# Performance work log

Hardware: AMD Instinct MI355X
Metric: run time of the kernel (lower is better)

## Reference

```python
import jax, jax.numpy as jnp
import numpy as np

DIM = 512
NUM_HEADS = 16
WS = 8  # window_size
N = WS * WS
B = 1024


def get_relative_index(h, w):
    coords_h = np.arange(h)[:, None].repeat(w, axis=1)
    coords_w = np.arange(w)[None, :].repeat(h, axis=0)
    coords = np.stack([coords_h, coords_w], axis=-1).reshape(-1, 2)  # [N,2]
    rel = coords[:, None, :] - coords[None, :, :]
    rel = rel + np.array([h - 1, w - 1])
    rel[:, :, 0] *= 2 * w - 1
    return rel.sum(-1).astype(np.int32)  # [N,N]


def setup_inputs() -> dict:
    key = jax.random.key(0)
    ks = jax.random.split(key, 6)
    table_size = (2 * WS - 1) * (2 * WS - 1)  # 225
    return {
        "x": jax.random.normal(ks[0], (B, N, DIM), dtype=jnp.float32),
        "qkv_weight": jax.random.normal(ks[1], (3 * DIM, DIM), dtype=jnp.float32) * 0.02,
        "qkv_bias": jax.random.normal(ks[2], (3 * DIM,), dtype=jnp.float32) * 0.02,
        "proj_weight": jax.random.normal(ks[3], (DIM, DIM), dtype=jnp.float32) * 0.02,
        "proj_bias": jax.random.normal(ks[4], (DIM,), dtype=jnp.float32) * 0.02,
        "relative_table": jax.random.normal(ks[5], (table_size, 2 * NUM_HEADS), dtype=jnp.float32) * 0.02,
        "relative_index": jnp.asarray(get_relative_index(WS, WS)),
    }


def reference(x, qkv_weight, qkv_bias, proj_weight, proj_bias, relative_table, relative_index):
    B_, n, C = x.shape
    H = NUM_HEADS
    hd = C // H
    scale = hd ** -0.5
    # qkv projection: [B,N,3C] -> [3,B,H,N,hd]
    qkv = (x @ qkv_weight.T + qkv_bias).reshape(B_, n, 3, H, hd).transpose(2, 0, 3, 1, 4)
    q, k, v = qkv[0], qkv[1], qkv[2]
    attn = jnp.einsum("bhnd,bhmd->bhnm", q * scale, k)  # [B,H,N,N]
    # learned relative-position bias + post-softmax scale
    params = relative_table[relative_index.reshape(-1)].reshape(n, n, 2 * H)
    params = params.transpose(2, 0, 1)  # [2H,N,N]
    rel_bias, rel_scale = params[:H], params[H:]
    attn = jax.nn.softmax(attn + rel_bias[None], axis=-1)
    attn = attn * rel_scale[None]
    out = jnp.einsum("bhnm,bhmd->bhnd", attn, v)
    out = out.transpose(0, 2, 1, 3).reshape(B_, n, C)
    return out @ proj_weight.T + proj_bias
```

## Files before the change

### kernel.cpp

```cpp
#include <hip/hip_runtime.h>

typedef unsigned short u16;
typedef unsigned int   u32;
typedef __attribute__((ext_vector_type(8))) short bf16x8;
typedef __attribute__((ext_vector_type(4))) float f32x4;

#define SCALE 0.17677669529663687f

__device__ __forceinline__ u16 f2bf(float f){
  u32 x = __float_as_uint(f);
  x += 0x7fffu + ((x >> 16) & 1u);
  return (u16)(x >> 16);
}
__device__ __forceinline__ float bf2f(u16 u){
  return __uint_as_float(((u32)u) << 16);
}


__global__ void prep_kernel(const float* __restrict__ qkvw, const float* __restrict__ projw,
                            const float* __restrict__ table, const int* __restrict__ relidx,
                            u16* __restrict__ qkvw_b, u16* __restrict__ projw_b,
                            u16* __restrict__ biasT, u16* __restrict__ scaleT){
  int i = blockIdx.x * 256 + threadIdx.x;
  if (i < 786432) {
    qkvw_b[i] = f2bf(qkvw[i]);
  } else if (i < 1048576) {
    int j = i - 786432; projw_b[j] = f2bf(projw[j]);
  } else if (i < 1114112) {
    int j = i - 1048576; int h = j >> 12, rc = j & 4095;
    int idx = relidx[rc];
    biasT [h*4096 + rc] = f2bf(table[idx*32 + h]);
    scaleT[h*4096 + rc] = f2bf(table[idx*32 + 16 + h]);
  }
}

__global__ void xconv_kernel(const float* __restrict__ x, u16* __restrict__ xb){
  size_t i = (size_t)blockIdx.x * 256 + threadIdx.x;
  const float4* xp = (const float4*)x;
  float4 a = xp[2*i], b = xp[2*i+1];
  union { u16 u[8]; uint4 v; } o;
  o.u[0]=f2bf(a.x); o.u[1]=f2bf(a.y); o.u[2]=f2bf(a.z); o.u[3]=f2bf(a.w);
  o.u[4]=f2bf(b.x); o.u[5]=f2bf(b.y); o.u[6]=f2bf(b.z); o.u[7]=f2bf(b.w);
  *(uint4*)(xb + 8*i) = o.v;
}

template<int EPI>
__global__ __launch_bounds__(512, 2) void gemm_kernel(
    const u16* __restrict__ A, const u16* __restrict__ W,
    const float* __restrict__ bias, void* __restrict__ outp, const int NT)
{
  __shared__ u16 lds[3][24576];
  const int tid = threadIdx.x, lane = tid & 63, wid = tid >> 6;
  const int wave_base = tid & ~63;

  const int cpx = gridDim.x >> 3;
  const int bid = (blockIdx.x & 7) * cpx + (blockIdx.x >> 3);
  const int mt = bid / NT, nt = bid % NT;
  const size_t m0 = (size_t)mt * 128;
  const int n0 = nt * 256;
  const int wm = wid >> 2, wn = wid & 3;
  const int NCOL = (EPI == 0) ? 1536 : 512;

  const f32x4 z = {0.f, 0.f, 0.f, 0.f};
  f32x4 acc[4][4];
#pragma unroll
  for (int i = 0; i < 4; i++)
#pragma unroll
    for (int j = 0; j < 4; j++) acc[i][j] = z;

  auto stage = [&](int ch){
    const int slot = ch % 3;
    const int kb = ch * 128;
    u16* base = &lds[slot][0];
#pragma unroll
    for (int c = 0; c < 2; ++c){
      const int t = c*512 + tid;
      const int row = t >> 3, sl = t & 7;
      const char* ga = (const char*)A + (m0 + row)*1024 + kb + ((sl ^ (row & 7)) << 4);
      u16* la = base + (size_t)(c*512 + wave_base)*8;
      __builtin_amdgcn_global_load_lds((const __attribute__((address_space(1))) u32*)ga,
                                       (__attribute__((address_space(3))) u32*)la, 16, 0, 0);
    }
#pragma unroll
    for (int c = 0; c < 4; ++c){
      const int t = c*512 + tid;
      const int col = t >> 3, sl = t & 7;
      const char* gb = (const char*)W + (size_t)(n0 + col)*1024 + kb + ((sl ^ (col & 7)) << 4);
      u16* lb = base + 8192 + (size_t)(c*512 + wave_base)*8;
      __builtin_amdgcn_global_load_lds((const __attribute__((address_space(1))) u32*)gb,
                                       (__attribute__((address_space(3))) u32*)lb, 16, 0, 0);
    }
  };

  auto compute = [&](int ch){
    const int slot = ch % 3;
    const u16* As = &lds[slot][0];
    const u16* Bs = &lds[slot][8192];
    bf16x8 af[2][4], bfr[2][4];
#pragma unroll
    for (int kk = 0; kk < 2; ++kk){
#pragma unroll
      for (int i = 0; i < 4; ++i){
        const int row = wm*64 + i*16 + (lane & 15);
        const int sa  = (kk*4 + (lane >> 4)) ^ (row & 7);
        af[kk][i] = *(const bf16x8*)&As[row*64 + sa*8];
        const int col = wn*64 + i*16 + (lane & 15);
        const int sb  = (kk*4 + (lane >> 4)) ^ (col & 7);
        bfr[kk][i] = *(const bf16x8*)&Bs[col*64 + sb*8];
      }
    }
    asm volatile("s_waitcnt lgkmcnt(0)" ::: "memory");
    __builtin_amdgcn_sched_barrier(0);
    __builtin_amdgcn_s_setprio(1);
#pragma unroll
    for (int kk = 0; kk < 2; ++kk)
#pragma unroll
      for (int i = 0; i < 4; ++i)
#pragma unroll
        for (int j = 0; j < 4; ++j)
          acc[i][j] = __builtin_amdgcn_mfma_f32_16x16x32_bf16(af[kk][i], bfr[kk][j], acc[i][j], 0, 0, 0);
    __builtin_amdgcn_s_setprio(0);
  };

  stage(0);
  stage(1);
  asm volatile("s_waitcnt vmcnt(6)" ::: "memory");
  __builtin_amdgcn_s_barrier();

#pragma unroll
  for (int ch = 0; ch < 8; ++ch){
    if (ch + 2 < 8) stage(ch + 2);
    compute(ch);
    if (ch < 7){
      if (ch + 2 < 8) { asm volatile("s_waitcnt vmcnt(6)" ::: "memory"); }
      else            { asm volatile("s_waitcnt vmcnt(0)" ::: "memory"); }
      __builtin_amdgcn_s_barrier();
    }
  }

  const int lr = (lane >> 4) << 2;
  const int lc = lane & 15;
  if (EPI == 0){
    u16* o = (u16*)outp;
#pragma unroll
    for (int j = 0; j < 4; ++j){
      const int col = n0 + wn*64 + j*16 + lc;
      const float bv = bias[col];
      const float sc = (col < 512) ? SCALE : 1.f;
#pragma unroll
      for (int i = 0; i < 4; ++i){
#pragma unroll
        for (int r = 0; r < 4; ++r){
          const size_t row = m0 + wm*64 + i*16 + lr + r;
          o[row*1536 + col] = f2bf((acc[i][j][r] + bv) * sc);
        }
      }
    }
  } else {
    float* o = (float*)outp;
#pragma unroll
    for (int j = 0; j < 4; ++j){
      const int col = n0 + wn*64 + j*16 + lc;
      const float bv = bias[col];
#pragma unroll
      for (int i = 0; i < 4; ++i){
#pragma unroll
        for (int r = 0; r < 4; ++r){
          const size_t row = m0 + wm*64 + i*16 + lr + r;
          o[row*512 + col] = acc[i][j][r] + bv;
        }
      }
    }
  }
}

__global__ __launch_bounds__(256) void attn_kernel(
    const u16* __restrict__ qkv, const u16* __restrict__ biasT,
    const u16* __restrict__ scaleT, u16* __restrict__ attn_out)
{
  __shared__ u16 qs[64*40];
  __shared__ u16 ks[64*40];
  __shared__ u16 vs[64*40];
  __shared__ u16 Ps[64*72];
  const int tid = threadIdx.x, lane = tid & 63, wid = tid >> 6;
  const int bh = blockIdx.x, b = bh >> 4, h = bh & 15;
  const u16* base = qkv + (size_t)b * 64 * 1536 + h * 32;
  {
    const int row = tid >> 2, seg = (tid & 3) * 8;
    const size_t ro = (size_t)row * 1536 + seg;
    *(uint4*)&qs[row*40 + seg] = *(const uint4*)(base + ro);
    *(uint4*)&ks[row*40 + seg] = *(const uint4*)(base + ro + 512);
    *(uint4*)&vs[row*40 + seg] = *(const uint4*)(base + ro + 1024);
  }
  __syncthreads();

  const int wr0 = wid * 16;
  const int lg = lane >> 4, lc = lane & 15;
  const f32x4 z = {0.f, 0.f, 0.f, 0.f};

  bf16x8 qf = *(const bf16x8*)&qs[(wr0 + lc)*40 + lg*8];
  f32x4 s[4];
#pragma unroll
  for (int ct = 0; ct < 4; ++ct){
    bf16x8 kf = *(const bf16x8*)&ks[(ct*16 + lc)*40 + lg*8];
    s[ct] = __builtin_amdgcn_mfma_f32_16x16x32_bf16(qf, kf, z, 0, 0, 0);
  }

  const u16* bT = biasT + h*4096;
  const u16* sT = scaleT + h*4096;
#pragma unroll
  for (int r = 0; r < 4; ++r){
    const int row = wr0 + lg*4 + r;
    float vals[4]; float mx = -1e30f;
#pragma unroll
    for (int ct = 0; ct < 4; ++ct){
      vals[ct] = s[ct][r] + bf2f(bT[row*64 + ct*16 + lc]);
      mx = fmaxf(mx, vals[ct]);
    }
    mx = fmaxf(mx, __shfl_xor(mx, 1));
    mx = fmaxf(mx, __shfl_xor(mx, 2));
    mx = fmaxf(mx, __shfl_xor(mx, 4));
    mx = fmaxf(mx, __shfl_xor(mx, 8));
    float sm = 0.f;
#pragma unroll
    for (int ct = 0; ct < 4; ++ct){ vals[ct] = __expf(vals[ct] - mx); sm += vals[ct]; }
    sm += __shfl_xor(sm, 1);
    sm += __shfl_xor(sm, 2);
    sm += __shfl_xor(sm, 4);
    sm += __shfl_xor(sm, 8);
    const float inv = 1.f / sm;
#pragma unroll
    for (int ct = 0; ct < 4; ++ct){
      const int col = ct*16 + lc;
      Ps[row*72 + col] = f2bf(vals[ct] * inv * bf2f(sT[row*64 + col]));
    }
  }
  __syncthreads();

  f32x4 o[2] = {z, z};
#pragma unroll
  for (int kc = 0; kc < 2; ++kc){
    bf16x8 pf = *(const bf16x8*)&Ps[(wr0 + lc)*72 + kc*32 + lg*8];
#pragma unroll
    for (int c2 = 0; c2 < 2; ++c2){
      union { u16 u[8]; bf16x8 v; } vf;
#pragma unroll
      for (int e = 0; e < 8; ++e)
        vf.u[e] = vs[(kc*32 + lg*8 + e)*40 + c2*16 + lc];
      o[c2] = __builtin_amdgcn_mfma_f32_16x16x32_bf16(pf, vf.v, o[c2], 0, 0, 0);
    }
  }

#pragma unroll
  for (int c2 = 0; c2 < 2; ++c2){
#pragma unroll
    for (int r = 0; r < 4; ++r){
      const int n = wr0 + lg*4 + r;
      attn_out[((size_t)b*64 + n)*512 + h*32 + c2*16 + lc] = f2bf(o[c2][r]);
    }
  }
}

extern "C" void kernel_launch(void* const* d_in, const int* in_sizes, int n_in,
                              void* d_out, int out_size, void* d_ws, size_t ws_size,
                              hipStream_t stream)
{
  const float* x      = (const float*)d_in[0];
  const float* qkvw   = (const float*)d_in[1];
  const float* qkvb   = (const float*)d_in[2];
  const float* projw  = (const float*)d_in[3];
  const float* projb  = (const float*)d_in[4];
  const float* table  = (const float*)d_in[5];
  const int*   relidx = (const int*)d_in[6];
  char* ws = (char*)d_ws;

  u16* qkvw_b = (u16*)(ws + 0);
  u16* projw_b= (u16*)(ws + 1572864);
  u16* biasT  = (u16*)(ws + 2097152);
  u16* scaleT = (u16*)(ws + 2228224);
  u16* qkvws  = (u16*)(ws + 2359296);
  u16* xb     = (u16*)(ws + 203685888);
  u16* attn_o = xb;

  if (ws_size < 270794752ull) return;

  prep_kernel<<<dim3(4352), dim3(256), 0, stream>>>(qkvw, projw, table, relidx,
                                                    qkvw_b, projw_b, biasT, scaleT);
  xconv_kernel<<<dim3(16384), dim3(256), 0, stream>>>(x, xb);
  gemm_kernel<0><<<dim3(3072), dim3(512), 0, stream>>>(xb, qkvw_b, qkvb, (void*)qkvws, 6);
  attn_kernel<<<dim3(16384), dim3(256), 0, stream>>>(qkvws, biasT, scaleT, attn_o);
  gemm_kernel<1><<<dim3(1024), dim3(512), 0, stream>>>(attn_o, projw_b, projb, d_out, 2);
}
```

Measured before the change: 302.0 us.

## Enlarge GEMM tile to 256x256 with split A/B staging per half-step

The GEMM kernel's output tile grows from 128x256 to 256x256, and the K chunk shrinks from 64 to 32, giving 16 chunks instead of 8. Each wave now computes two 64x64 sub-tiles, and the A and B loads are staged in separate phases that are interleaved with the two MFMA groups. Both GEMM grids are halved to match. The aim is more data reuse per LDS load and fewer blocks. The cost is double the accumulator registers under the same launch bounds, which risks spilling or lower occupancy. It also adds more barriers per chunk and drops the XOR swizzle on the LDS layout, which may bring back bank conflicts.

New measurement: 330.3 us. 9.4% more time.

```diff
diff --git a/kernel.cpp b/kernel.cpp
--- a/kernel.cpp
+++ b/kernel.cpp
@@ -49,93 +49,98 @@
     const u16* __restrict__ A, const u16* __restrict__ W,
     const float* __restrict__ bias, void* __restrict__ outp, const int NT)
 {
-  __shared__ u16 lds[3][24576];
+  __shared__ u16 lds[3][16384];
   const int tid = threadIdx.x, lane = tid & 63, wid = tid >> 6;
   const int wave_base = tid & ~63;
 
   const int cpx = gridDim.x >> 3;
   const int bid = (blockIdx.x & 7) * cpx + (blockIdx.x >> 3);
   const int mt = bid / NT, nt = bid % NT;
-  const size_t m0 = (size_t)mt * 128;
+  const size_t m0 = (size_t)mt * 256;
   const int n0 = nt * 256;
   const int wm = wid >> 2, wn = wid & 3;
-  const int NCOL = (EPI == 0) ? 1536 : 512;
 
   const f32x4 z = {0.f, 0.f, 0.f, 0.f};
-  f32x4 acc[4][4];
-#pragma unroll
-  for (int i = 0; i < 4; i++)
+  f32x4 acc[8][4];
+#pragma unroll
+  for (int i = 0; i < 8; i++)
 #pragma unroll
     for (int j = 0; j < 4; j++) acc[i][j] = z;
 
-  auto stage = [&](int ch){
+  auto stageA = [&](int ch){
     const int slot = ch % 3;
-    const int kb = ch * 128;
-    u16* base = &lds[slot][0];
+    const int kb = ch * 32;
 #pragma unroll
     for (int c = 0; c < 2; ++c){
       const int t = c*512 + tid;
-      const int row = t >> 3, sl = t & 7;
-      const char* ga = (const char*)A + (m0 + row)*1024 + kb + ((sl ^ (row & 7)) << 4);
-      u16* la = base + (size_t)(c*512 + wave_base)*8;
+      const int row = t >> 2, sl = t & 3;
+      const u16* ga = A + (m0 + row)*512 + kb + sl*8;
+      u16* la = &lds[slot][(size_t)(c*512 + wave_base)*8];
       __builtin_amdgcn_global_load_lds((const __attribute__((address_space(1))) u32*)ga,
                                        (__attribute__((address_space(3))) u32*)la, 16, 0, 0);
     }
-#pragma unroll
-    for (int c = 0; c < 4; ++c){
+  };
+  auto stageB = [&](int ch){
+    const int slot = ch % 3;
+    const int kb = ch * 32;
+#pragma unroll
+    for (int c = 0; c < 2; ++c){
       const int t = c*512 + tid;
-      const int col = t >> 3, sl = t & 7;
-      const char* gb = (const char*)W + (size_t)(n0 + col)*1024 + kb + ((sl ^ (col & 7)) << 4);
-      u16* lb = base + 8192 + (size_t)(c*512 + wave_base)*8;
+      const int col = t >> 2, sl = t & 3;
+      const u16* gb = W + (size_t)(n0 + col)*512 + kb + sl*8;
+      u16* lb = &lds[slot][8192 + (size_t)(c*512 + wave_base)*8];
       __builtin_amdgcn_global_load_lds((const __attribute__((address_space(1))) u32*)gb,
                                        (__attribute__((address_space(3))) u32*)lb, 16, 0, 0);
     }
   };
 
-  auto compute = [&](int ch){
+  stageA(0); stageB(0);
+  stageA(1); stageB(1);
+  asm volatile("s_waitcnt vmcnt(4)" ::: "memory");
+  __builtin_amdgcn_s_barrier();
+
+#pragma unroll
+  for (int ch = 0; ch < 16; ++ch){
     const int slot = ch % 3;
     const u16* As = &lds[slot][0];
     const u16* Bs = &lds[slot][8192];
-    bf16x8 af[2][4], bfr[2][4];
-#pragma unroll
-    for (int kk = 0; kk < 2; ++kk){
-#pragma unroll
-      for (int i = 0; i < 4; ++i){
-        const int row = wm*64 + i*16 + (lane & 15);
-        const int sa  = (kk*4 + (lane >> 4)) ^ (row & 7);
-        af[kk][i] = *(const bf16x8*)&As[row*64 + sa*8];
-        const int col = wn*64 + i*16 + (lane & 15);
-        const int sb  = (kk*4 + (lane >> 4)) ^ (col & 7);
-        bfr[kk][i] = *(const bf16x8*)&Bs[col*64 + sb*8];
-      }
-    }
+    bf16x8 af[4], bfr[4], af2[4];
+
+#pragma unroll
+    for (int i = 0; i < 4; ++i){
+      af[i]  = *(const bf16x8*)&As[(wm*128 + i*16 + (lane&15))*32 + ((lane>>4)<<3)];
+      bfr[i] = *(const bf16x8*)&Bs[(wn*64  + i*16 + (lane&15))*32 + ((lane>>4)<<3)];
+    }
+    if (ch + 2 < 16) stageA(ch + 2);
+    __builtin_amdgcn_s_barrier();
     asm volatile("s_waitcnt lgkmcnt(0)" ::: "memory");
     __builtin_amdgcn_sched_barrier(0);
     __builtin_amdgcn_s_setprio(1);
 #pragma unroll
-    for (int kk = 0; kk < 2; ++kk)
-#pragma unroll
-      for (int i = 0; i < 4; ++i)
-#pragma unroll
-        for (int j = 0; j < 4; ++j)
-          acc[i][j] = __builtin_amdgcn_mfma_f32_16x16x32_bf16(af[kk][i], bfr[kk][j], acc[i][j], 0, 0, 0);
+    for (int i = 0; i < 4; ++i)
+#pragma unroll
+      for (int j = 0; j < 4; ++j)
+        acc[i][j] = __builtin_amdgcn_mfma_f32_16x16x32_bf16(af[i], bfr[j], acc[i][j], 0, 0, 0);
     __builtin_amdgcn_s_setprio(0);
-  };
-
-  stage(0);
-  stage(1);
-  asm volatile("s_waitcnt vmcnt(6)" ::: "memory");
-  __builtin_amdgcn_s_barrier();
-
-#pragma unroll
-  for (int ch = 0; ch < 8; ++ch){
-    if (ch + 2 < 8) stage(ch + 2);
-    compute(ch);
-    if (ch < 7){
-      if (ch + 2 < 8) { asm volatile("s_waitcnt vmcnt(6)" ::: "memory"); }
-      else            { asm volatile("s_waitcnt vmcnt(0)" ::: "memory"); }
-      __builtin_amdgcn_s_barrier();
-    }
+    __builtin_amdgcn_s_barrier();
+
+#pragma unroll
+    for (int i = 0; i < 4; ++i)
+      af2[i] = *(const bf16x8*)&As[(wm*128 + 64 + i*16 + (lane&15))*32 + ((lane>>4)<<3)];
+    if (ch + 2 < 16) stageB(ch + 2);
+    __builtin_amdgcn_s_barrier();
+    asm volatile("s_waitcnt lgkmcnt(0)" ::: "memory");
+    __builtin_amdgcn_sched_barrier(0);
+    __builtin_amdgcn_s_setprio(1);
+#pragma unroll
+    for (int i = 0; i < 4; ++i)
+#pragma unroll
+      for (int j = 0; j < 4; ++j)
+        acc[4+i][j] = __builtin_amdgcn_mfma_f32_16x16x32_bf16(af2[i], bfr[j], acc[4+i][j], 0, 0, 0);
+    __builtin_amdgcn_s_setprio(0);
+    if (ch < 14)       { asm volatile("s_waitcnt vmcnt(4)" ::: "memory"); }
+    else if (ch == 14) { asm volatile("s_waitcnt vmcnt(0)" ::: "memory"); }
+    if (ch < 15) __builtin_amdgcn_s_barrier();
   }
 
   const int lr = (lane >> 4) << 2;
@@ -143,31 +148,31 @@
   if (EPI == 0){
     u16* o = (u16*)outp;
 #pragma unroll
-    for (int j = 0; j < 4; ++j){
-      const int col = n0 + wn*64 + j*16 + lc;
+    for (int nf = 0; nf < 4; ++nf){
+      const int col = n0 + wn*64 + nf*16 + lc;
       const float bv = bias[col];
       const float sc = (col < 512) ? SCALE : 1.f;
 #pragma unroll
-      for (int i = 0; i < 4; ++i){
+      for (int mf = 0; mf < 8; ++mf){
 #pragma unroll
         for (int r = 0; r < 4; ++r){
-          const size_t row = m0 + wm*64 + i*16 + lr + r;
-          o[row*1536 + col] = f2bf((acc[i][j][r] + bv) * sc);
+          const size_t row = m0 + wm*128 + mf*16 + lr + r;
+          o[row*1536 + col] = f2bf((acc[mf][nf][r] + bv) * sc);
         }
       }
     }
   } else {
     float* o = (float*)outp;
 #pragma unroll
-    for (int j = 0; j < 4; ++j){
-      const int col = n0 + wn*64 + j*16 + lc;
+    for (int nf = 0; nf < 4; ++nf){
+      const int col = n0 + wn*64 + nf*16 + lc;
       const float bv = bias[col];
 #pragma unroll
-      for (int i = 0; i < 4; ++i){
+      for (int mf = 0; mf < 8; ++mf){
 #pragma unroll
         for (int r = 0; r < 4; ++r){
-          const size_t row = m0 + wm*64 + i*16 + lr + r;
-          o[row*512 + col] = acc[i][j][r] + bv;
+          const size_t row = m0 + wm*128 + mf*16 + lr + r;
+          o[row*512 + col] = acc[mf][nf][r] + bv;
         }
       }
     }
@@ -287,7 +292,7 @@
   prep_kernel<<<dim3(4352), dim3(256), 0, stream>>>(qkvw, projw, table, relidx,
                                                     qkvw_b, projw_b, biasT, scaleT);
   xconv_kernel<<<dim3(16384), dim3(256), 0, stream>>>(x, xb);
-  gemm_kernel<0><<<dim3(3072), dim3(512), 0, stream>>>(xb, qkvw_b, qkvb, (void*)qkvws, 6);
+  gemm_kernel<0><<<dim3(1536), dim3(512), 0, stream>>>(xb, qkvw_b, qkvb, (void*)qkvws, 6);
   attn_kernel<<<dim3(16384), dim3(256), 0, stream>>>(qkvws, biasT, scaleT, attn_o);
-  gemm_kernel<1><<<dim3(1024), dim3(512), 0, stream>>>(attn_o, projw_b, projb, d_out, 2);
-}
+  gemm_kernel<1><<<dim3(512), dim3(512), 0, stream>>>(attn_o, projw_b, projb, d_out, 2);
+}
```
